# Kernel optimization log

Hardware: AMD Instinct MI355X
Metric: run time of the kernel (lower is better)

## Reference

```python
import jax, jax.numpy as jnp
import numpy as np

L, B, E = 8192, 2, 1024
H, WS = 16, 256
D = E // H


def setup_inputs() -> dict:
    key = jax.random.key(0)
    ks = jax.random.split(key, 8)
    mk = lambda k: jax.random.normal(k, (E, E), dtype=jnp.float32) * 0.02
    return {
        'query': jax.random.normal(ks[0], (L, B, E), dtype=jnp.float32),
        'key':   jax.random.normal(ks[1], (L, B, E), dtype=jnp.float32),
        'value': jax.random.normal(ks[2], (L, B, E), dtype=jnp.float32),
        'Wq': mk(ks[3]), 'bq': jnp.zeros((E,), jnp.float32),
        'Wk': mk(ks[4]), 'bk': jnp.zeros((E,), jnp.float32),
        'Wv': mk(ks[5]), 'bv': jnp.zeros((E,), jnp.float32),
        'Wo': mk(ks[6]), 'bo': jnp.zeros((E,), jnp.float32),
    }


def reference(query, key, value, Wq, bq, Wk, bk, Wv, bv, Wo, bo):
    # Faithful translation, including the original's (B,L,H,D) layout and the
    # raw-memory view(B,H,L//ws,ws,D) reinterpretation of that layout.
    proj = lambda x, W, b: x @ W.T + b
    # (L,B,E) -> (L,B,H,D) -> transpose(0,1) -> (B,L,H,D)
    q = jnp.swapaxes(proj(query, Wq, bq).reshape(L, B, H, D), 0, 1)
    k = jnp.swapaxes(proj(key,   Wk, bk).reshape(L, B, H, D), 0, 1)
    v = jnp.swapaxes(proj(value, Wv, bv).reshape(L, B, H, D), 0, 1)
    # L > ws, L % ws == 0 -> pad_len = 0; contiguous().view == reshape
    nW = L // WS
    q = q.reshape(B, H, nW, WS, D)
    k = k.reshape(B, H, nW, WS, D)
    v = v.reshape(B, H, nW, WS, D)
    attn = jnp.einsum('bhnqd,bhnkd->bhnqk', q, k) / (D ** 0.5)
    attn = jax.nn.softmax(attn, axis=-1)
    out = jnp.einsum('bhnqk,bhnkd->bhnqd', attn, v)  # (B,H,nW,ws,D)
    out = out.reshape(B, H, L, D)
    # transpose(0,1).contiguous().view(L,B,E): reinterpret (H,B,L,D) memory
    out = jnp.swapaxes(out, 0, 1).reshape(L, B, E)
    return out @ Wo.T + bo
```

## Files before the change

### kernel.cpp

```cpp
#include <hip/hip_runtime.h>


typedef _Float16 half8 __attribute__((ext_vector_type(8)));
typedef _Float16 half4 __attribute__((ext_vector_type(4)));
typedef float    f32x4 __attribute__((ext_vector_type(4)));

#define MFMA16(a, b, c) __builtin_amdgcn_mfma_f32_16x16x32_f16((a), (b), (c), 0, 0, 0)

__device__ inline void gload16(const _Float16* g, _Float16* l) {
  __builtin_amdgcn_global_load_lds(
      (const __attribute__((address_space(1))) void*)g,
      (__attribute__((address_space(3))) void*)l, 16, 0, 0);
}

__device__ inline half8 cvt8(float4 a, float4 b) {
  half8 h = {(_Float16)a.x, (_Float16)a.y, (_Float16)a.z, (_Float16)a.w,
             (_Float16)b.x, (_Float16)b.y, (_Float16)b.z, (_Float16)b.w};
  return h;
}

__global__ __launch_bounds__(256) void cvtw_k(const float* __restrict__ s0,
                                              const float* __restrict__ s1,
                                              const float* __restrict__ s2,
                                              const float* __restrict__ s3,
                                              _Float16* __restrict__ d) {
  const float* s = blockIdx.y == 0 ? s0 : blockIdx.y == 1 ? s1 : blockIdx.y == 2 ? s2 : s3;
  _Float16* dst = d + (size_t)blockIdx.y * (1 << 20);
  int i = (blockIdx.x * 256 + threadIdx.x) * 8;
  float4 a = *(const float4*)(s + i);
  float4 b = *(const float4*)(s + i + 4);
  *(half8*)(dst + i) = cvt8(a, b);
}

template <int A_F32, int OUT_F32>
__device__ __attribute__((always_inline)) void gemm_body(
    const void* __restrict__ A, const _Float16* __restrict__ Bw,
    const float* __restrict__ bias, void* __restrict__ Cout, int m0, int n0) {
  constexpr int K = 1024, N = 1024, NT = 16;
  __shared__ alignas(16) _Float16 As[2][128 * 64];
  __shared__ alignas(16) _Float16 Bs[2][128 * 64];
  const int tid = threadIdx.x, lane = tid & 63, wave = tid >> 6;
  const int r15 = lane & 15, g = lane >> 4;
  const int wr = wave >> 1, wc = wave & 1;

  const int srow = lane >> 3, kc = lane & 7;
  const int scol = (kc ^ srow) * 8;

  f32x4 acc[4][4] = {};

  if (A_F32) {
#pragma unroll
    for (int i = 0; i < 4; i++) {
      int q = i * 4 + wave;
      const float* s = (const float*)A + (size_t)(m0 + q * 8 + srow) * K + kc * 8;
      float4 f0 = *(const float4*)s, f1 = *(const float4*)(s + 4);
      *(half8*)&As[0][q * 512 + srow * 64 + ((kc ^ srow) * 8)] = cvt8(f0, f1);
    }
  } else {
#pragma unroll
    for (int i = 0; i < 4; i++) {
      int q = i * 4 + wave;
      gload16((const _Float16*)A + (size_t)(m0 + q * 8 + srow) * K + scol, &As[0][q * 512]);
    }
  }
#pragma unroll
  for (int i = 0; i < 4; i++) {
    int q = i * 4 + wave;
    gload16(Bw + (size_t)(n0 + q * 8 + srow) * K + scol, &Bs[0][q * 512]);
  }
  __syncthreads();

  int cur = 0;
  for (int t = 0; t < NT; t++) {
    const int nxt = cur ^ 1;
    const bool pf = (t + 1 < NT);
    float4 fr[8];
    if (pf) {
      if (A_F32) {
#pragma unroll
        for (int i = 0; i < 4; i++) {
          int q = i * 4 + wave;
          const float* s =
              (const float*)A + (size_t)(m0 + q * 8 + srow) * K + (t + 1) * 64 + kc * 8;
          fr[i * 2] = *(const float4*)s;
          fr[i * 2 + 1] = *(const float4*)(s + 4);
        }
      } else {
#pragma unroll
        for (int i = 0; i < 4; i++) {
          int q = i * 4 + wave;
          gload16((const _Float16*)A + (size_t)(m0 + q * 8 + srow) * K + (t + 1) * 64 + scol,
                  &As[nxt][q * 512]);
        }
      }
#pragma unroll
      for (int i = 0; i < 4; i++) {
        int q = i * 4 + wave;
        gload16(Bw + (size_t)(n0 + q * 8 + srow) * K + (t + 1) * 64 + scol,
                &Bs[nxt][q * 512]);
      }
    }
    __builtin_amdgcn_sched_barrier(0);

    half8 af[4][2], bf[4][2];
#pragma unroll
    for (int mi = 0; mi < 4; mi++) {
      int row = wr * 64 + mi * 16 + r15;
#pragma unroll
      for (int kk = 0; kk < 2; kk++)
        af[mi][kk] = *(half8*)&As[cur][row * 64 + (((kk * 4 + g) ^ (row & 7)) * 8)];
    }
#pragma unroll
    for (int ni = 0; ni < 4; ni++) {
      int row = wc * 64 + ni * 16 + r15;
#pragma unroll
      for (int kk = 0; kk < 2; kk++)
        bf[ni][kk] = *(half8*)&Bs[cur][row * 64 + (((kk * 4 + g) ^ (row & 7)) * 8)];
    }
#pragma unroll
    for (int kk = 0; kk < 2; kk++)
#pragma unroll
      for (int mi = 0; mi < 4; mi++)
#pragma unroll
        for (int ni = 0; ni < 4; ni++)
          acc[mi][ni] = MFMA16(af[mi][kk], bf[ni][kk], acc[mi][ni]);
    __builtin_amdgcn_sched_barrier(0);

    if (pf && A_F32) {
#pragma unroll
      for (int i = 0; i < 4; i++) {
        int q = i * 4 + wave;
        *(half8*)&As[nxt][q * 512 + srow * 64 + ((kc ^ srow) * 8)] =
            cvt8(fr[i * 2], fr[i * 2 + 1]);
      }
    }
    __syncthreads();
    cur = nxt;
  }

#pragma unroll
  for (int ni = 0; ni < 4; ni++) {
    const int col = n0 + wc * 64 + ni * 16 + r15;
    const float bv = bias[col];
#pragma unroll
    for (int mi = 0; mi < 4; mi++) {
      const int rowb = m0 + wr * 64 + mi * 16 + g * 4;
#pragma unroll
      for (int r = 0; r < 4; r++) {
        float x = acc[mi][ni][r] + bv;
        if (OUT_F32)
          ((float*)Cout)[(size_t)(rowb + r) * N + col] = x;
        else
          ((_Float16*)Cout)[(size_t)(rowb + r) * N + col] = (_Float16)x;
      }
    }
  }
}

__global__ __launch_bounds__(256) void gemm_proj_k(
    const float* __restrict__ Aq, const float* __restrict__ Ak,
    const float* __restrict__ Av, const _Float16* __restrict__ W16,
    const float* __restrict__ bq, const float* __restrict__ bk,
    const float* __restrict__ bv, _Float16* __restrict__ Oq,
    _Float16* __restrict__ Ok, _Float16* __restrict__ Ov) {
  const int z = blockIdx.z;
  const float* A = z == 0 ? Aq : z == 1 ? Ak : Av;
  const float* bias = z == 0 ? bq : z == 1 ? bk : bv;
  _Float16* out = z == 0 ? Oq : z == 1 ? Ok : Ov;
  gemm_body<1, 0>((const void*)A, W16 + ((size_t)z << 20), bias, (void*)out,
                  blockIdx.x * 128, blockIdx.y * 128);
}

__global__ __launch_bounds__(256) void gemm_out_k(const _Float16* __restrict__ A,
                                                  const _Float16* __restrict__ Bw,
                                                  const float* __restrict__ bias,
                                                  float* __restrict__ Cout) {
  gemm_body<0, 1>((const void*)A, Bw, bias, (void*)Cout, blockIdx.x * 128,
                  blockIdx.y * 128);
}

__global__ __launch_bounds__(256) void vtrans_k(const _Float16* __restrict__ Vp,
                                                _Float16* __restrict__ Vt) {
  const int c = blockIdx.x, b = blockIdx.y;
  __shared__ alignas(16) _Float16 Vl[256 * 64];
  const int tid = threadIdx.x;
  const int l0 = c * 16;
#pragma unroll
  for (int i = 0; i < 8; i++) {
    int q = tid + i * 256;
    int w = q >> 3, ck = q & 7;
    int ls = l0 + (w >> 4), h = w & 15;
    half8 v = *(const half8*)(Vp + (size_t)(ls * 2 + b) * 1024 + h * 64 + ck * 8);
    *(half8*)&Vl[w * 64 + (ck ^ (w & 7)) * 8] = v;
  }
  __syncthreads();
  const int d = tid >> 2, kcq = tid & 3;
  const size_t obase = ((size_t)(b * 512 + c) * 64 + d) * 256 + kcq * 64;
#pragma unroll
  for (int i8 = 0; i8 < 8; i8++) {
    half8 v;
#pragma unroll
    for (int j = 0; j < 8; j++) {
      int k = kcq * 64 + i8 * 8 + j;
      v[j] = Vl[k * 64 + (((d >> 3) ^ (k & 7)) * 8) + (d & 7)];
    }
    *(half8*)(Vt + obase + i8 * 8) = v;
  }
}

__global__ __launch_bounds__(512) void attn_win_k(const _Float16* __restrict__ Qp,
                                                  const _Float16* __restrict__ Kp,
                                                  const _Float16* __restrict__ Vt,
                                                  _Float16* __restrict__ Y) {
  const int c = blockIdx.x, b = blockIdx.y;
  __shared__ alignas(16) _Float16 Kl[256 * 64];
  __shared__ alignas(16) _Float16 Vl[64 * 256];
  const int tid = threadIdx.x, lane = tid & 63, wave = tid >> 6;
  const int i15 = lane & 15, g = lane >> 4;
  const int l0 = c * 16;

#pragma unroll
  for (int i = 0; i < 4; i++) {
    int q = tid + i * 512;
    int w = q >> 3, ck = q & 7;
    int ls = l0 + (w >> 4), h = w & 15;
    half8 v = *(const half8*)(Kp + (size_t)(ls * 2 + b) * 1024 + h * 64 + ck * 8);
    *(half8*)&Kl[w * 64 + (ck ^ (w & 7)) * 8] = v;
  }
  const size_t vb0 = (size_t)(b * 512 + c) * 64 * 256;
#pragma unroll
  for (int i = 0; i < 4; i++) {
    int q = tid + i * 512;
    int d = q >> 5, ck = q & 31;
    half8 v = *(const half8*)(Vt + vb0 + (size_t)d * 256 + ck * 8);
    *(half8*)&Vl[d * 256 + (ck ^ ((d & 7) << 2)) * 8] = v;
  }
  half8 qf[2][2];
#pragma unroll
  for (int wf = 0; wf < 2; wf++)
#pragma unroll
    for (int dh = 0; dh < 2; dh++) {
      int ls = l0 + wave * 2 + wf;
      qf[wf][dh] =
          *(const half8*)(Qp + (size_t)(ls * 2 + b) * 1024 + i15 * 64 + dh * 32 + g * 8);
    }
  __syncthreads();

  f32x4 acc[16][2] = {};
#pragma unroll
  for (int m = 0; m < 16; m++) {
    int row = m * 16 + i15;
    half8 a0 = *(half8*)&Kl[row * 64 + ((g) ^ (i15 & 7)) * 8];
    half8 a1 = *(half8*)&Kl[row * 64 + ((4 + g) ^ (i15 & 7)) * 8];
    acc[m][0] = MFMA16(a0, qf[0][0], acc[m][0]);
    acc[m][0] = MFMA16(a1, qf[0][1], acc[m][0]);
    acc[m][1] = MFMA16(a0, qf[1][0], acc[m][1]);
    acc[m][1] = MFMA16(a1, qf[1][1], acc[m][1]);
  }

#pragma unroll
  for (int wf = 0; wf < 2; wf++) {
    float mx = -3.0e38f;
#pragma unroll
    for (int m = 0; m < 16; m++)
#pragma unroll
      for (int r = 0; r < 4; r++) mx = fmaxf(mx, acc[m][wf][r]);
    mx = fmaxf(mx, __shfl_xor(mx, 16, 64));
    mx = fmaxf(mx, __shfl_xor(mx, 32, 64));
    float sum = 0.f;
#pragma unroll
    for (int m = 0; m < 16; m++)
#pragma unroll
      for (int r = 0; r < 4; r++) {
        float e = __expf((acc[m][wf][r] - mx) * 0.125f);
        acc[m][wf][r] = e;
        sum += e;
      }
    sum += __shfl_xor(sum, 16, 64);
    sum += __shfl_xor(sum, 32, 64);
    float inv = 1.f / sum;
#pragma unroll
    for (int m = 0; m < 16; m++)
#pragma unroll
      for (int r = 0; r < 4; r++) acc[m][wf][r] *= inv;
  }
  __syncthreads();

  _Float16* Pw = &Kl[wave * 2048];
  f32x4 oacc[2][4] = {};
#pragma unroll
  for (int kq = 0; kq < 4; kq++) {
#pragma unroll
    for (int wf = 0; wf < 2; wf++) {
      int rrow = wf * 16 + i15;
#pragma unroll
      for (int ml = 0; ml < 4; ml++) {
        f32x4 pv = acc[kq * 4 + ml][wf];
        half4 h = {(_Float16)pv[0], (_Float16)pv[1], (_Float16)pv[2], (_Float16)pv[3]};
        int ck = ml * 2 + (g >> 1);
        *(half4*)&Pw[rrow * 64 + ((ck ^ (i15 & 7)) * 8) + (g & 1) * 4] = h;
      }
    }
    asm volatile("s_waitcnt lgkmcnt(0)" ::: "memory");
    __builtin_amdgcn_sched_barrier(0);
#pragma unroll
    for (int kfl = 0; kfl < 2; kfl++) {
      half8 pa0 = *(half8*)&Pw[(i15)*64 + (((kfl * 4 + g) ^ (i15 & 7)) * 8)];
      half8 pa1 = *(half8*)&Pw[(16 + i15) * 64 + (((kfl * 4 + g) ^ (i15 & 7)) * 8)];
#pragma unroll
      for (int df = 0; df < 4; df++) {
        int drow = df * 16 + i15;
        half8 vbf =
            *(half8*)&Vl[drow * 256 + (((kq * 8 + kfl * 4 + g) ^ ((i15 & 7) << 2)) * 8)];
        oacc[0][df] = MFMA16(pa0, vbf, oacc[0][df]);
        oacc[1][df] = MFMA16(pa1, vbf, oacc[1][df]);
      }
    }
  }

  const int h2 = c >> 5, n = c & 31;
  const size_t yb = ((size_t)(h2 * 2 + b) * 8192 + (size_t)n * 256) * 64;
#pragma unroll
  for (int wf = 0; wf < 2; wf++)
#pragma unroll
    for (int df = 0; df < 4; df++)
#pragma unroll
      for (int r = 0; r < 4; r++) {
        int w = wave * 32 + wf * 16 + g * 4 + r;
        Y[yb + (size_t)w * 64 + df * 16 + i15] = (_Float16)oacc[wf][df][r];
      }
}

extern "C" void kernel_launch(void* const* d_in, const int* in_sizes, int n_in,
                              void* d_out, int out_size, void* d_ws, size_t ws_size,
                              hipStream_t stream) {
  const float* query = (const float*)d_in[0];
  const float* key_ = (const float*)d_in[1];
  const float* value = (const float*)d_in[2];
  const float* Wq = (const float*)d_in[3];
  const float* bq = (const float*)d_in[4];
  const float* Wk = (const float*)d_in[5];
  const float* bk = (const float*)d_in[6];
  const float* Wv = (const float*)d_in[7];
  const float* bv = (const float*)d_in[8];
  const float* Wo = (const float*)d_in[9];
  const float* bo = (const float*)d_in[10];

  _Float16* ws = (_Float16*)d_ws;
  _Float16* W16 = ws;
  _Float16* W16o = W16 + 3 * (1 << 20);
  _Float16* Vp = ws + 4 * (1 << 20);
  _Float16* Vt = Vp + (1 << 24);
  _Float16* Ybuf = Vp;

  _Float16* Qp = (_Float16*)d_out;
  _Float16* Kp = Qp + (1 << 24);

  cvtw_k<<<dim3(512, 4), 256, 0, stream>>>(Wq, Wk, Wv, Wo, W16);

  gemm_proj_k<<<dim3(128, 8, 3), 256, 0, stream>>>(query, key_, value, W16, bq, bk, bv,
                                                   Qp, Kp, Vp);

  vtrans_k<<<dim3(512, 2), 256, 0, stream>>>(Vp, Vt);
  attn_win_k<<<dim3(512, 2), 512, 0, stream>>>(Qp, Kp, Vt, Ybuf);

  gemm_out_k<<<dim3(128, 8), 256, 0, stream>>>(Ybuf, W16o, bo, (float*)d_out);

  (void)in_sizes; (void)n_in; (void)out_size; (void)ws_size;
}
```

Baseline: 315.3 us.

## Rewrite projection GEMMs as 256x256-tile, 8-wave kernels with split-K-half pipelining

Replaces the 128x128, 4-wave GEMM body with a 256x256 tile computed by 8 waves (512 threads). Each wave accumulates 128x64, which raises operand reuse per LDS load. The 64-wide K step is split into two 32-wide halves held in a packed, swizzled LDS layout using 128KB of shared memory. Loads for the next step are interleaved between MFMA groups using explicit vmcnt/lgkmcnt waits, raw barriers and setprio, with the fp32-to-fp16 conversion of A overlapped the same way. The trade-off is fewer blocks (768 and 256) and heavy LDS and register use, which may hurt occupancy and tail balance on the output GEMM.

```diff
diff --git a/kernel.cpp b/kernel.cpp
--- a/kernel.cpp
+++ b/kernel.cpp
@@ -6,6 +6,10 @@
 typedef float    f32x4 __attribute__((ext_vector_type(4)));
 
 #define MFMA16(a, b, c) __builtin_amdgcn_mfma_f32_16x16x32_f16((a), (b), (c), 0, 0, 0)
+#define VM(n) asm volatile("s_waitcnt vmcnt(" #n ")" ::: "memory")
+#define SCHED0 __builtin_amdgcn_sched_barrier(0)
+#define LGKM0 do { asm volatile("s_waitcnt lgkmcnt(0)" ::: "memory"); SCHED0; } while (0)
+#define BARW do { __builtin_amdgcn_s_barrier(); SCHED0; } while (0)
 
 __device__ inline void gload16(const _Float16* g, _Float16* l) {
   __builtin_amdgcn_global_load_lds(
@@ -33,109 +37,167 @@
 }
 
 template <int A_F32, int OUT_F32>
-__device__ __attribute__((always_inline)) void gemm_body(
+__device__ __attribute__((always_inline)) void gemm8p_body(
     const void* __restrict__ A, const _Float16* __restrict__ Bw,
-    const float* __restrict__ bias, void* __restrict__ Cout, int m0, int n0) {
-  constexpr int K = 1024, N = 1024, NT = 16;
-  __shared__ alignas(16) _Float16 As[2][128 * 64];
-  __shared__ alignas(16) _Float16 Bs[2][128 * 64];
+    const float* __restrict__ bias, void* __restrict__ Cout) {
+  constexpr int K = 1024, NN = 1024, NT = 16;
+  __shared__ alignas(16) _Float16 SH[65536];
   const int tid = threadIdx.x, lane = tid & 63, wave = tid >> 6;
   const int r15 = lane & 15, g = lane >> 4;
-  const int wr = wave >> 1, wc = wave & 1;
-
-  const int srow = lane >> 3, kc = lane & 7;
-  const int scol = (kc ^ srow) * 8;
-
-  f32x4 acc[4][4] = {};
+  const int wr = wave >> 2, wc = wave & 3;
+  const int m0 = blockIdx.x * 256, n0 = blockIdx.y * 256;
+
+  const int sp = tid >> 3;
+  const int sv = (tid & 7) ^ (sp & 7);
+  const int srow = 2 * sp + (sv >> 2);
+  const int scol = (sv & 3) * 8;
+  const int sdst = tid * 8;
+
+  const int rp = r15 >> 1, rsub = r15 & 1;
+  const int rslot = ((rsub * 4 + g) ^ rp) * 8;
+
+  const float* Af = (const float*)A;
+  const _Float16* Ah = (const _Float16*)A;
+
+  f32x4 acc[8][4] = {};
+  float4 fr0[4], fr1[4];
+  half8 af[4], bf[4];
+
+#define A_REGION(buf, kh) (&SH[(buf)*16384 + (kh)*8192])
+#define B_REGION(buf, kh) (&SH[32768 + (buf)*16384 + (kh)*8192])
+
+#define STAGE_B(t, buf, kh)                                                    \
+  do {                                                                         \
+    const _Float16* _s = Bw + (size_t)(n0 + srow) * K + (t)*64 + (kh)*32 + scol; \
+    gload16(_s, B_REGION(buf, kh) + sdst);                                     \
+    gload16(_s + (size_t)128 * K, B_REGION(buf, kh) + sdst + 4096);            \
+  } while (0)
+
+#define STAGE_A16(t, buf, kh)                                                  \
+  do {                                                                         \
+    const _Float16* _s = Ah + (size_t)(m0 + srow) * K + (t)*64 + (kh)*32 + scol; \
+    gload16(_s, A_REGION(buf, kh) + sdst);                                     \
+    gload16(_s + (size_t)128 * K, A_REGION(buf, kh) + sdst + 4096);            \
+  } while (0)
+
+#define A_ISSUE(fr, t, kh)                                                     \
+  do {                                                                         \
+    const float* _s = Af + (size_t)(m0 + srow) * K + (t)*64 + (kh)*32 + scol;  \
+    fr[0] = ((const float4*)_s)[0];                                            \
+    fr[1] = ((const float4*)_s)[1];                                            \
+    const float* _s2 = _s + (size_t)128 * K;                                   \
+    fr[2] = ((const float4*)_s2)[0];                                           \
+    fr[3] = ((const float4*)_s2)[1];                                           \
+  } while (0)
+
+#define A_WRITE(fr, buf, kh)                                                   \
+  do {                                                                         \
+    *(half8*)&A_REGION(buf, kh)[sdst] = cvt8(fr[0], fr[1]);                    \
+    *(half8*)&A_REGION(buf, kh)[sdst + 4096] = cvt8(fr[2], fr[3]);             \
+  } while (0)
+
+#define READ_AF(buf, kk, MH)                                                   \
+  do {                                                                         \
+    _Float16* _b = A_REGION(buf, kk);                                          \
+    int _pb = (wr * 64 + (MH)*32 + rp) * 64 + rslot;                           \
+    af[0] = *(half8*)&_b[_pb];                                                 \
+    af[1] = *(half8*)&_b[_pb + 512];                                           \
+    af[2] = *(half8*)&_b[_pb + 1024];                                          \
+    af[3] = *(half8*)&_b[_pb + 1536];                                          \
+  } while (0)
+
+#define READ_BF(buf, kk)                                                       \
+  do {                                                                         \
+    _Float16* _b = B_REGION(buf, kk);                                          \
+    int _pb = (wc * 32 + rp) * 64 + rslot;                                     \
+    bf[0] = *(half8*)&_b[_pb];                                                 \
+    bf[1] = *(half8*)&_b[_pb + 512];                                           \
+    bf[2] = *(half8*)&_b[_pb + 1024];                                          \
+    bf[3] = *(half8*)&_b[_pb + 1536];                                          \
+  } while (0)
+
+#define MFMA_Q(MH)                                                             \
+  do {                                                                         \
+    __builtin_amdgcn_s_setprio(1);                                             \
+    _Pragma("unroll") for (int mi = 0; mi < 4; mi++)                           \
+        _Pragma("unroll") for (int ni = 0; ni < 4; ni++) acc[(MH)*4 + mi][ni] = \
+        MFMA16(af[mi], bf[ni], acc[(MH)*4 + mi][ni]);                          \
+    __builtin_amdgcn_s_setprio(0);                                             \
+  } while (0)
 
   if (A_F32) {
-#pragma unroll
-    for (int i = 0; i < 4; i++) {
-      int q = i * 4 + wave;
-      const float* s = (const float*)A + (size_t)(m0 + q * 8 + srow) * K + kc * 8;
-      float4 f0 = *(const float4*)s, f1 = *(const float4*)(s + 4);
-      *(half8*)&As[0][q * 512 + srow * 64 + ((kc ^ srow) * 8)] = cvt8(f0, f1);
-    }
+    A_ISSUE(fr0, 0, 0);
+    A_ISSUE(fr1, 0, 1);
+    STAGE_B(0, 0, 0);
+    STAGE_B(0, 0, 1);
+    VM(8); SCHED0;
+    A_WRITE(fr0, 0, 0);
+    VM(4); SCHED0;
+    A_WRITE(fr1, 0, 1);
+    asm volatile("s_waitcnt lgkmcnt(0)" ::: "memory");
   } else {
-#pragma unroll
-    for (int i = 0; i < 4; i++) {
-      int q = i * 4 + wave;
-      gload16((const _Float16*)A + (size_t)(m0 + q * 8 + srow) * K + scol, &As[0][q * 512]);
-    }
-  }
-#pragma unroll
-  for (int i = 0; i < 4; i++) {
-    int q = i * 4 + wave;
-    gload16(Bw + (size_t)(n0 + q * 8 + srow) * K + scol, &Bs[0][q * 512]);
-  }
-  __syncthreads();
-
-  int cur = 0;
-  for (int t = 0; t < NT; t++) {
-    const int nxt = cur ^ 1;
-    const bool pf = (t + 1 < NT);
-    float4 fr[8];
-    if (pf) {
-      if (A_F32) {
-#pragma unroll
-        for (int i = 0; i < 4; i++) {
-          int q = i * 4 + wave;
-          const float* s =
-              (const float*)A + (size_t)(m0 + q * 8 + srow) * K + (t + 1) * 64 + kc * 8;
-          fr[i * 2] = *(const float4*)s;
-          fr[i * 2 + 1] = *(const float4*)(s + 4);
-        }
-      } else {
-#pragma unroll
-        for (int i = 0; i < 4; i++) {
-          int q = i * 4 + wave;
-          gload16((const _Float16*)A + (size_t)(m0 + q * 8 + srow) * K + (t + 1) * 64 + scol,
-                  &As[nxt][q * 512]);
-        }
-      }
-#pragma unroll
-      for (int i = 0; i < 4; i++) {
-        int q = i * 4 + wave;
-        gload16(Bw + (size_t)(n0 + q * 8 + srow) * K + (t + 1) * 64 + scol,
-                &Bs[nxt][q * 512]);
-      }
-    }
-    __builtin_amdgcn_sched_barrier(0);
-
-    half8 af[4][2], bf[4][2];
-#pragma unroll
-    for (int mi = 0; mi < 4; mi++) {
-      int row = wr * 64 + mi * 16 + r15;
-#pragma unroll
-      for (int kk = 0; kk < 2; kk++)
-        af[mi][kk] = *(half8*)&As[cur][row * 64 + (((kk * 4 + g) ^ (row & 7)) * 8)];
-    }
-#pragma unroll
-    for (int ni = 0; ni < 4; ni++) {
-      int row = wc * 64 + ni * 16 + r15;
-#pragma unroll
-      for (int kk = 0; kk < 2; kk++)
-        bf[ni][kk] = *(half8*)&Bs[cur][row * 64 + (((kk * 4 + g) ^ (row & 7)) * 8)];
-    }
-#pragma unroll
-    for (int kk = 0; kk < 2; kk++)
-#pragma unroll
-      for (int mi = 0; mi < 4; mi++)
-#pragma unroll
-        for (int ni = 0; ni < 4; ni++)
-          acc[mi][ni] = MFMA16(af[mi][kk], bf[ni][kk], acc[mi][ni]);
-    __builtin_amdgcn_sched_barrier(0);
-
-    if (pf && A_F32) {
-#pragma unroll
-      for (int i = 0; i < 4; i++) {
-        int q = i * 4 + wave;
-        *(half8*)&As[nxt][q * 512 + srow * 64 + ((kc ^ srow) * 8)] =
-            cvt8(fr[i * 2], fr[i * 2 + 1]);
-      }
-    }
-    __syncthreads();
-    cur = nxt;
+    STAGE_A16(0, 0, 0);
+    STAGE_A16(0, 0, 1);
+    STAGE_B(0, 0, 0);
+    STAGE_B(0, 0, 1);
+  }
+
+  for (int t = 0; t < NT - 1; t++) {
+    const int buf = t & 1, nb = buf ^ 1;
+    if (A_F32) {
+      A_ISSUE(fr0, t + 1, 0);
+      VM(6);
+    } else {
+      STAGE_A16(t + 1, nb, 0);
+      VM(4);
+    }
+    BARW;
+    READ_AF(buf, 0, 0);
+    READ_BF(buf, 0);
+    LGKM0;
+    MFMA_Q(0);
+    if (A_F32) A_ISSUE(fr1, t + 1, 1);
+    else STAGE_A16(t + 1, nb, 1);
+    READ_AF(buf, 0, 1);
+    LGKM0;
+    MFMA_Q(1);
+    STAGE_B(t + 1, nb, 0);
+    VM(6); SCHED0;
+    if (A_F32) A_WRITE(fr0, nb, 0);
+    BARW;
+    READ_AF(buf, 1, 0);
+    READ_BF(buf, 1);
+    LGKM0;
+    MFMA_Q(0);
+    STAGE_B(t + 1, nb, 1);
+    if (A_F32) {
+      VM(4); SCHED0;
+      A_WRITE(fr1, nb, 1);
+    }
+    READ_AF(buf, 1, 1);
+    LGKM0;
+    MFMA_Q(1);
+  }
+
+  {
+    VM(2);
+    BARW;
+    READ_AF(1, 0, 0);
+    READ_BF(1, 0);
+    LGKM0;
+    MFMA_Q(0);
+    READ_AF(1, 0, 1);
+    LGKM0;
+    MFMA_Q(1);
+    VM(0);
+    BARW;
+    READ_AF(1, 1, 0);
+    READ_BF(1, 1);
+    LGKM0;
+    MFMA_Q(0);
+    READ_AF(1, 1, 1);
+    LGKM0;
+    MFMA_Q(1);
   }
 
 #pragma unroll
@@ -143,21 +205,30 @@
     const int col = n0 + wc * 64 + ni * 16 + r15;
     const float bv = bias[col];
 #pragma unroll
-    for (int mi = 0; mi < 4; mi++) {
-      const int rowb = m0 + wr * 64 + mi * 16 + g * 4;
+    for (int mi8 = 0; mi8 < 8; mi8++) {
+      const int rowb = m0 + wr * 128 + mi8 * 16 + g * 4;
 #pragma unroll
       for (int r = 0; r < 4; r++) {
-        float x = acc[mi][ni][r] + bv;
+        float x = acc[mi8][ni][r] + bv;
         if (OUT_F32)
-          ((float*)Cout)[(size_t)(rowb + r) * N + col] = x;
+          ((float*)Cout)[(size_t)(rowb + r) * NN + col] = x;
         else
-          ((_Float16*)Cout)[(size_t)(rowb + r) * N + col] = (_Float16)x;
+          ((_Float16*)Cout)[(size_t)(rowb + r) * NN + col] = (_Float16)x;
       }
     }
   }
-}
-
-__global__ __launch_bounds__(256) void gemm_proj_k(
+#undef A_REGION
+#undef B_REGION
+#undef STAGE_B
+#undef STAGE_A16
+#undef A_ISSUE
+#undef A_WRITE
+#undef READ_AF
+#undef READ_BF
+#undef MFMA_Q
+}
+
+__global__ __launch_bounds__(512) void gemm_proj_k(
     const float* __restrict__ Aq, const float* __restrict__ Ak,
     const float* __restrict__ Av, const _Float16* __restrict__ W16,
     const float* __restrict__ bq, const float* __restrict__ bk,
@@ -167,16 +238,14 @@
   const float* A = z == 0 ? Aq : z == 1 ? Ak : Av;
   const float* bias = z == 0 ? bq : z == 1 ? bk : bv;
   _Float16* out = z == 0 ? Oq : z == 1 ? Ok : Ov;
-  gemm_body<1, 0>((const void*)A, W16 + ((size_t)z << 20), bias, (void*)out,
-                  blockIdx.x * 128, blockIdx.y * 128);
-}
-
-__global__ __launch_bounds__(256) void gemm_out_k(const _Float16* __restrict__ A,
+  gemm8p_body<1, 0>((const void*)A, W16 + ((size_t)z << 20), bias, (void*)out);
+}
+
+__global__ __launch_bounds__(512) void gemm_out_k(const _Float16* __restrict__ A,
                                                   const _Float16* __restrict__ Bw,
                                                   const float* __restrict__ bias,
                                                   float* __restrict__ Cout) {
-  gemm_body<0, 1>((const void*)A, Bw, bias, (void*)Cout, blockIdx.x * 128,
-                  blockIdx.y * 128);
+  gemm8p_body<0, 1>((const void*)A, Bw, bias, (void*)Cout);
 }
 
 __global__ __launch_bounds__(256) void vtrans_k(const _Float16* __restrict__ Vp,
@@ -358,13 +427,13 @@
 
   cvtw_k<<<dim3(512, 4), 256, 0, stream>>>(Wq, Wk, Wv, Wo, W16);
 
-  gemm_proj_k<<<dim3(128, 8, 3), 256, 0, stream>>>(query, key_, value, W16, bq, bk, bv,
-                                                   Qp, Kp, Vp);
+  gemm_proj_k<<<dim3(64, 4, 3), 512, 0, stream>>>(query, key_, value, W16, bq, bk, bv,
+                                                  Qp, Kp, Vp);
 
   vtrans_k<<<dim3(512, 2), 256, 0, stream>>>(Vp, Vt);
   attn_win_k<<<dim3(512, 2), 512, 0, stream>>>(Qp, Kp, Vt, Ybuf);
 
-  gemm_out_k<<<dim3(128, 8), 256, 0, stream>>>(Ybuf, W16o, bo, (float*)d_out);
+  gemm_out_k<<<dim3(64, 4), 512, 0, stream>>>(Ybuf, W16o, bo, (float*)d_out);
 
   (void)in_sizes; (void)n_in; (void)out_size; (void)ws_size;
 }
```

New measurement: 255.0 us. 1.24x faster.
